# Kernel tuning notes

Measured on AMD Instinct MI355X. Metric: run time of the kernel, lower is better.

## Reference

```python
import jax, jax.numpy as jnp
import numpy as np


def setup_inputs() -> dict:
    key = jax.random.key(0)
    k1, k2 = jax.random.split(key)
    B, N, M = 32, 4096, 4096
    pred = jax.random.normal(k1, (B, N, 3), dtype=jnp.float32)
    target = jax.random.normal(k2, (B, M, 3), dtype=jnp.float32)
    return {"pred": pred, "target": target}


def reference(pred, target):
    # pairwise euclidean distances: [B, N, M]
    # d2 = |p|^2 + |t|^2 - 2 p.t  (matches torch.cdist p=2)
    p2 = jnp.sum(pred * pred, axis=-1)                      # [B, N]
    t2 = jnp.sum(target * target, axis=-1)                  # [B, M]
    pt = jnp.einsum('bnd,bmd->bnm', pred, target)           # [B, N, M]
    d2 = p2[:, :, None] + t2[:, None, :] - 2.0 * pt
    dist = jnp.sqrt(jnp.maximum(d2, 0.0))                   # [B, N, M]
    min_d = jnp.min(dist, axis=2)                           # [B, N]
    return jnp.mean(min_d)
```

## Files before the change

### kernel.cpp

```cpp
#include <hip/hip_runtime.h>


typedef short bf16x8 __attribute__((ext_vector_type(8)));
typedef float f32x16 __attribute__((ext_vector_type(16)));

constexpr int Bc = 32;
constexpr int Nc = 4096;
constexpr int Mc = 4096;
constexpr int BLOCK = 256;
constexpr int PTS = Bc * Nc;
constexpr int S = 4;
constexpr int TPB = 1024;
constexpr int PPB = 512;
constexpr unsigned POISON = 0xAAAAAAAAu;

__device__ __forceinline__ unsigned short brne(float x) {
  unsigned u = __float_as_uint(x);
  return (unsigned short)((u + 0x7FFFu + ((u >> 16) & 1u)) >> 16);
}
__device__ __forceinline__ float bf2f(unsigned short h) {
  return __uint_as_float(((unsigned)h) << 16);
}
__device__ __forceinline__ unsigned pack(unsigned short lo, unsigned short hi) {
  return (unsigned)lo | ((unsigned)hi << 16);
}

__global__ __launch_bounds__(BLOCK)
__attribute__((amdgpu_waves_per_eu(4, 4)))
void emd_fused_kernel(const float* __restrict__ pred,
                      const float* __restrict__ target,
                      unsigned* __restrict__ minb,
                      unsigned* __restrict__ cnts,
                      float* __restrict__ out) {
  __shared__ uint4 lds[2048];

  const int pg = blockIdx.x >> 2;
  const int s = blockIdx.x & 3;
  const int b = pg >> 3;
  const int lane = threadIdx.x & 63;
  const int half = lane >> 5;
  const int l31 = lane & 31;
  const int wave = threadIdx.x >> 6;
  const unsigned short ONE = 0x3F80;

  float pld[2][3];
#pragma unroll
  for (int j = 0; j < 2; ++j) {
    const size_t gi = (size_t)pg * PPB + threadIdx.x + j * BLOCK;
    pld[j][0] = pred[3 * gi];
    pld[j][1] = pred[3 * gi + 1];
    pld[j][2] = pred[3 * gi + 2];
  }
  const size_t tbase = (size_t)b * Mc + s * TPB;
  const float4* tp4 = (const float4*)(target + tbase * 3);
  float4 f0 = tp4[3 * threadIdx.x + 0];
  float4 f1 = tp4[3 * threadIdx.x + 1];
  float4 f2 = tp4[3 * threadIdx.x + 2];

#pragma unroll
  for (int j = 0; j < 2; ++j) {
    const int p = threadIdx.x + j * BLOCK;
    float x = pld[j][0], y = pld[j][1], z = pld[j][2];
    unsigned short xh = brne(x), xl = brne(x - bf2f(xh));
    unsigned short yh = brne(y), yl = brne(y - bf2f(yh));
    unsigned short zh = brne(z), zl = brne(z - bf2f(zh));
    float p2 = fmaf(x, x, fmaf(y, y, z * z));
    unsigned short ph = brne(p2), pl = brne(p2 - bf2f(ph));
    lds[p] = make_uint4(pack(xh, xl), pack(xh, yh), pack(yl, yh), pack(zh, zl));
    lds[512 + p] = make_uint4(pack(zh, ONE), pack(ONE, ph), pack(pl, 0), 0);
  }

  uint4 t0[4];
  {
    float cx[4] = {f0.x, f0.w, f1.z, f2.y};
    float cy[4] = {f0.y, f1.x, f1.w, f2.z};
    float cz[4] = {f0.z, f1.y, f2.x, f2.w};
#pragma unroll
    for (int j = 0; j < 4; ++j) {
      const int pt = 4 * threadIdx.x + j;
      float X = -2.0f * cx[j], Y = -2.0f * cy[j], Z = -2.0f * cz[j];
      unsigned short Xh = brne(X), Xl = brne(X - bf2f(Xh));
      unsigned short Yh = brne(Y), Yl = brne(Y - bf2f(Yh));
      unsigned short Zh = brne(Z), Zl = brne(Z - bf2f(Zh));
      float t2 = 0.25f * fmaf(X, X, fmaf(Y, Y, Z * Z));
      unsigned short th = brne(t2), tl = brne(t2 - bf2f(th));
      t0[j] =
          make_uint4(pack(Xh, Xh), pack(Xl, Yh), pack(Yh, Yl), pack(Zh, Zh));
      lds[1024 + pt] =
          make_uint4(pack(Zl, th), pack(tl, ONE), pack(ONE, 0), 0);
    }
  }
  __syncthreads();

  bf16x8 bfr[4];
#pragma unroll
  for (int f = 0; f < 4; ++f) {
    uint4 u = lds[half * 512 + wave * 128 + f * 32 + l31];
    bfr[f] = *(const bf16x8*)&u;
  }
  __syncthreads();

#pragma unroll
  for (int j = 0; j < 4; ++j) lds[4 * threadIdx.x + j] = t0[j];
  __syncthreads();

  float rA[4], rB[4];
#pragma unroll
  for (int f = 0; f < 4; ++f) { rA[f] = 3.4e38f; rB[f] = 3.4e38f; }

  const int abase = half * 1024 + l31;
#pragma unroll 2
  for (int t = 0; t < 32; ++t) {
    uint4 au = lds[abase + t * 32];
    bf16x8 af = *(const bf16x8*)&au;
    f32x16 z{};
    f32x16 d0 = __builtin_amdgcn_mfma_f32_32x32x16_bf16(af, bfr[0], z, 0, 0, 0);
    f32x16 d1 = __builtin_amdgcn_mfma_f32_32x32x16_bf16(af, bfr[1], z, 0, 0, 0);
    f32x16 d2 = __builtin_amdgcn_mfma_f32_32x32x16_bf16(af, bfr[2], z, 0, 0, 0);
    f32x16 d3 = __builtin_amdgcn_mfma_f32_32x32x16_bf16(af, bfr[3], z, 0, 0, 0);
#pragma unroll
    for (int i = 0; i < 16; i += 4) {
      rA[0] = fminf(fminf(d0[i], d0[i + 1]), rA[0]);
      rB[0] = fminf(fminf(d0[i + 2], d0[i + 3]), rB[0]);
      rA[1] = fminf(fminf(d1[i], d1[i + 1]), rA[1]);
      rB[1] = fminf(fminf(d1[i + 2], d1[i + 3]), rB[1]);
      rA[2] = fminf(fminf(d2[i], d2[i + 1]), rA[2]);
      rB[2] = fminf(fminf(d2[i + 2], d2[i + 3]), rB[2]);
      rA[3] = fminf(fminf(d3[i], d3[i + 1]), rA[3]);
      rB[3] = fminf(fminf(d3[i + 2], d3[i + 3]), rB[3]);
    }
  }

  const unsigned gbase = (unsigned)pg * PPB + wave * 128;
#pragma unroll
  for (int f = 0; f < 4; ++f) {
    float rr = fminf(rA[f], rB[f]);
    rr = fminf(rr, __shfl_xor(rr, 32, 64));
    if (lane < 32)
      __hip_atomic_fetch_min(&minb[gbase + f * 32 + l31],
                             __float_as_uint(fmaxf(rr, 0.0f)),
                             __ATOMIC_RELAXED, __HIP_MEMORY_SCOPE_AGENT);
  }

  asm volatile("s_waitcnt vmcnt(0)" ::: "memory");
  __syncthreads();

  unsigned* lflag = (unsigned*)lds;
  if (threadIdx.x == 0) {
    unsigned old = __hip_atomic_fetch_add(&cnts[pg], 1u, __ATOMIC_RELAXED,
                                          __HIP_MEMORY_SCOPE_AGENT);
    lflag[0] = (old == POISON + 3u || old == 3u) ? 1u : 0u;
  }
  __syncthreads();
  if (lflag[0]) {
    float ssum = 0.0f;
    const unsigned base = (unsigned)pg * PPB;
#pragma unroll
    for (int i = threadIdx.x; i < PPB; i += BLOCK) {
      unsigned ub = __hip_atomic_load(&minb[base + i], __ATOMIC_RELAXED,
                                      __HIP_MEMORY_SCOPE_AGENT);
      ssum += sqrtf(__uint_as_float(ub));
    }
#pragma unroll
    for (int off = 32; off > 0; off >>= 1) ssum += __shfl_down(ssum, off, 64);
    float* lsum = (float*)lds;
    if ((threadIdx.x & 63) == 0) lsum[1 + (threadIdx.x >> 6)] = ssum;
    __syncthreads();
    if (threadIdx.x == 0) {
      float tot = (lsum[1] + lsum[2]) + (lsum[3] + lsum[4]);
      atomicAdd(out, tot * (1.0f / (float)PTS));
    }
  }
}

extern "C" void kernel_launch(void* const* d_in, const int* in_sizes, int n_in,
                              void* d_out, int out_size, void* d_ws, size_t ws_size,
                              hipStream_t stream) {
  const float* pred = (const float*)d_in[0];
  const float* target = (const float*)d_in[1];
  unsigned* minb = (unsigned*)d_ws;
  unsigned* cnts = minb + PTS;
  emd_fused_kernel<<<dim3((PTS / PPB) * S), dim3(BLOCK), 0, stream>>>(
      pred, target, minb, cnts, (float*)d_out);
}
```

Before: 73.36 us.

## Split target range into eight slices, halve LDS, swizzle LDS indices

```diff
diff --git a/kernel.cpp b/kernel.cpp
--- a/kernel.cpp
+++ b/kernel.cpp
@@ -9,8 +9,8 @@
 constexpr int Mc = 4096;
 constexpr int BLOCK = 256;
 constexpr int PTS = Bc * Nc;
-constexpr int S = 4;
-constexpr int TPB = 1024;
+constexpr int S = 8;
+constexpr int TPB = 512;
 constexpr int PPB = 512;
 constexpr unsigned POISON = 0xAAAAAAAAu;
 
@@ -24,42 +24,64 @@
 __device__ __forceinline__ unsigned pack(unsigned short lo, unsigned short hi) {
   return (unsigned)lo | ((unsigned)hi << 16);
 }
+__device__ __forceinline__ int SW(int s) {
+  return s ^ ((s >> 3) & 7);
+}
 
 __global__ __launch_bounds__(BLOCK)
-__attribute__((amdgpu_waves_per_eu(4, 4)))
+__attribute__((amdgpu_waves_per_eu(8, 8)))
 void emd_fused_kernel(const float* __restrict__ pred,
                       const float* __restrict__ target,
                       unsigned* __restrict__ minb,
                       unsigned* __restrict__ cnts,
                       float* __restrict__ out) {
-  __shared__ uint4 lds[2048];
+  __shared__ uint4 lds[1024];
 
-  const int pg = blockIdx.x >> 2;
-  const int s = blockIdx.x & 3;
+  const int pg = blockIdx.x >> 3;
+  const int s = blockIdx.x & 7;
   const int b = pg >> 3;
   const int lane = threadIdx.x & 63;
   const int half = lane >> 5;
   const int l31 = lane & 31;
   const int wave = threadIdx.x >> 6;
+  const int tid = threadIdx.x;
   const unsigned short ONE = 0x3F80;
 
   float pld[2][3];
 #pragma unroll
   for (int j = 0; j < 2; ++j) {
-    const size_t gi = (size_t)pg * PPB + threadIdx.x + j * BLOCK;
+    const size_t gi = (size_t)pg * PPB + tid + j * BLOCK;
     pld[j][0] = pred[3 * gi];
     pld[j][1] = pred[3 * gi + 1];
     pld[j][2] = pred[3 * gi + 2];
   }
   const size_t tbase = (size_t)b * Mc + s * TPB;
-  const float4* tp4 = (const float4*)(target + tbase * 3);
-  float4 f0 = tp4[3 * threadIdx.x + 0];
-  float4 f1 = tp4[3 * threadIdx.x + 1];
-  float4 f2 = tp4[3 * threadIdx.x + 2];
+  const float2* tp2 = (const float2*)(target + tbase * 3);
+  float2 g0 = tp2[3 * tid + 0];
+  float2 g1 = tp2[3 * tid + 1];
+  float2 g2 = tp2[3 * tid + 2];
+
+  uint4 t0[2], t1[2];
+  {
+    float cx[2] = {g0.x, g1.y};
+    float cy[2] = {g0.y, g2.x};
+    float cz[2] = {g1.x, g2.y};
+#pragma unroll
+    for (int j = 0; j < 2; ++j) {
+      float X = -2.0f * cx[j], Y = -2.0f * cy[j], Z = -2.0f * cz[j];
+      unsigned short Xh = brne(X), Xl = brne(X - bf2f(Xh));
+      unsigned short Yh = brne(Y), Yl = brne(Y - bf2f(Yh));
+      unsigned short Zh = brne(Z), Zl = brne(Z - bf2f(Zh));
+      float t2 = 0.25f * fmaf(X, X, fmaf(Y, Y, Z * Z));
+      unsigned short th = brne(t2), tl = brne(t2 - bf2f(th));
+      t0[j] = make_uint4(pack(Xh, Xh), pack(Xl, Yh), pack(Yh, Yl), pack(Zh, Zh));
+      t1[j] = make_uint4(pack(Zl, th), pack(tl, ONE), pack(ONE, 0), 0);
+    }
+  }
 
 #pragma unroll
   for (int j = 0; j < 2; ++j) {
-    const int p = threadIdx.x + j * BLOCK;
+    const int p = tid + j * BLOCK;
     float x = pld[j][0], y = pld[j][1], z = pld[j][2];
     unsigned short xh = brne(x), xl = brne(x - bf2f(xh));
     unsigned short yh = brne(y), yl = brne(y - bf2f(yh));
@@ -68,27 +90,6 @@
     unsigned short ph = brne(p2), pl = brne(p2 - bf2f(ph));
     lds[p] = make_uint4(pack(xh, xl), pack(xh, yh), pack(yl, yh), pack(zh, zl));
     lds[512 + p] = make_uint4(pack(zh, ONE), pack(ONE, ph), pack(pl, 0), 0);
-  }
-
-  uint4 t0[4];
-  {
-    float cx[4] = {f0.x, f0.w, f1.z, f2.y};
-    float cy[4] = {f0.y, f1.x, f1.w, f2.z};
-    float cz[4] = {f0.z, f1.y, f2.x, f2.w};
-#pragma unroll
-    for (int j = 0; j < 4; ++j) {
-      const int pt = 4 * threadIdx.x + j;
-      float X = -2.0f * cx[j], Y = -2.0f * cy[j], Z = -2.0f * cz[j];
-      unsigned short Xh = brne(X), Xl = brne(X - bf2f(Xh));
-      unsigned short Yh = brne(Y), Yl = brne(Y - bf2f(Yh));
-      unsigned short Zh = brne(Z), Zl = brne(Z - bf2f(Zh));
-      float t2 = 0.25f * fmaf(X, X, fmaf(Y, Y, Z * Z));
-      unsigned short th = brne(t2), tl = brne(t2 - bf2f(th));
-      t0[j] =
-          make_uint4(pack(Xh, Xh), pack(Xl, Yh), pack(Yh, Yl), pack(Zh, Zh));
-      lds[1024 + pt] =
-          make_uint4(pack(Zl, th), pack(tl, ONE), pack(ONE, 0), 0);
-    }
   }
   __syncthreads();
 
@@ -101,17 +102,20 @@
   __syncthreads();
 
 #pragma unroll
-  for (int j = 0; j < 4; ++j) lds[4 * threadIdx.x + j] = t0[j];
+  for (int j = 0; j < 2; ++j) {
+    lds[SW(2 * tid + j)] = t0[j];
+    lds[SW(512 + 2 * tid + j)] = t1[j];
+  }
   __syncthreads();
 
   float rA[4], rB[4];
 #pragma unroll
   for (int f = 0; f < 4; ++f) { rA[f] = 3.4e38f; rB[f] = 3.4e38f; }
 
-  const int abase = half * 1024 + l31;
+  const int abase = half * 512 + l31;
 #pragma unroll 2
-  for (int t = 0; t < 32; ++t) {
-    uint4 au = lds[abase + t * 32];
+  for (int t = 0; t < 16; ++t) {
+    uint4 au = lds[SW(abase + t * 32)];
     bf16x8 af = *(const bf16x8*)&au;
     f32x16 z{};
     f32x16 d0 = __builtin_amdgcn_mfma_f32_32x32x16_bf16(af, bfr[0], z, 0, 0, 0);
@@ -146,17 +150,17 @@
   __syncthreads();
 
   unsigned* lflag = (unsigned*)lds;
-  if (threadIdx.x == 0) {
+  if (tid == 0) {
     unsigned old = __hip_atomic_fetch_add(&cnts[pg], 1u, __ATOMIC_RELAXED,
                                           __HIP_MEMORY_SCOPE_AGENT);
-    lflag[0] = (old == POISON + 3u || old == 3u) ? 1u : 0u;
+    lflag[0] = (old == POISON + (S - 1) || old == (unsigned)(S - 1)) ? 1u : 0u;
   }
   __syncthreads();
   if (lflag[0]) {
     float ssum = 0.0f;
     const unsigned base = (unsigned)pg * PPB;
 #pragma unroll
-    for (int i = threadIdx.x; i < PPB; i += BLOCK) {
+    for (int i = tid; i < PPB; i += BLOCK) {
       unsigned ub = __hip_atomic_load(&minb[base + i], __ATOMIC_RELAXED,
                                       __HIP_MEMORY_SCOPE_AGENT);
       ssum += sqrtf(__uint_as_float(ub));
@@ -164,9 +168,9 @@
 #pragma unroll
     for (int off = 32; off > 0; off >>= 1) ssum += __shfl_down(ssum, off, 64);
     float* lsum = (float*)lds;
-    if ((threadIdx.x & 63) == 0) lsum[1 + (threadIdx.x >> 6)] = ssum;
+    if ((tid & 63) == 0) lsum[1 + (tid >> 6)] = ssum;
     __syncthreads();
-    if (threadIdx.x == 0) {
+    if (tid == 0) {
       float tot = (lsum[1] + lsum[2]) + (lsum[3] + lsum[4]);
       atomicAdd(out, tot * (1.0f / (float)PTS));
     }
```

Result: slower. 76.80 us (+4.7%).

## Double block to 512 threads, halving per-wave B fragments and MFMAs

Applied to the files above, without the earlier changes.

```diff
diff --git a/kernel.cpp b/kernel.cpp
--- a/kernel.cpp
+++ b/kernel.cpp
@@ -7,7 +7,7 @@
 constexpr int Bc = 32;
 constexpr int Nc = 4096;
 constexpr int Mc = 4096;
-constexpr int BLOCK = 256;
+constexpr int BLOCK = 512;
 constexpr int PTS = Bc * Nc;
 constexpr int S = 4;
 constexpr int TPB = 1024;
@@ -26,7 +26,7 @@
 }
 
 __global__ __launch_bounds__(BLOCK)
-__attribute__((amdgpu_waves_per_eu(4, 4)))
+__attribute__((amdgpu_waves_per_eu(8, 8)))
 void emd_fused_kernel(const float* __restrict__ pred,
                       const float* __restrict__ target,
                       unsigned* __restrict__ minb,
@@ -41,72 +41,65 @@
   const int half = lane >> 5;
   const int l31 = lane & 31;
   const int wave = threadIdx.x >> 6;
+  const int tid = threadIdx.x;
   const unsigned short ONE = 0x3F80;
 
-  float pld[2][3];
+  float px, py, pz;
+  {
+    const size_t gi = (size_t)pg * PPB + tid;
+    px = pred[3 * gi]; py = pred[3 * gi + 1]; pz = pred[3 * gi + 2];
+  }
+  const size_t tbase = (size_t)b * Mc + s * TPB;
+  float tx[2], ty[2], tz[2];
 #pragma unroll
   for (int j = 0; j < 2; ++j) {
-    const size_t gi = (size_t)pg * PPB + threadIdx.x + j * BLOCK;
-    pld[j][0] = pred[3 * gi];
-    pld[j][1] = pred[3 * gi + 1];
-    pld[j][2] = pred[3 * gi + 2];
+    const size_t ti = tbase + tid + j * 512;
+    tx[j] = target[3 * ti]; ty[j] = target[3 * ti + 1];
+    tz[j] = target[3 * ti + 2];
   }
-  const size_t tbase = (size_t)b * Mc + s * TPB;
-  const float4* tp4 = (const float4*)(target + tbase * 3);
-  float4 f0 = tp4[3 * threadIdx.x + 0];
-  float4 f1 = tp4[3 * threadIdx.x + 1];
-  float4 f2 = tp4[3 * threadIdx.x + 2];
 
+  uint4 t0[2];
 #pragma unroll
   for (int j = 0; j < 2; ++j) {
-    const int p = threadIdx.x + j * BLOCK;
-    float x = pld[j][0], y = pld[j][1], z = pld[j][2];
+    float X = -2.0f * tx[j], Y = -2.0f * ty[j], Z = -2.0f * tz[j];
+    unsigned short Xh = brne(X), Xl = brne(X - bf2f(Xh));
+    unsigned short Yh = brne(Y), Yl = brne(Y - bf2f(Yh));
+    unsigned short Zh = brne(Z), Zl = brne(Z - bf2f(Zh));
+    float t2 = 0.25f * fmaf(X, X, fmaf(Y, Y, Z * Z));
+    unsigned short th = brne(t2), tl = brne(t2 - bf2f(th));
+    t0[j] = make_uint4(pack(Xh, Xh), pack(Xl, Yh), pack(Yh, Yl), pack(Zh, Zh));
+    lds[1024 + tid + j * 512] =
+        make_uint4(pack(Zl, th), pack(tl, ONE), pack(ONE, 0), 0);
+  }
+
+  {
+    float x = px, y = py, z = pz;
     unsigned short xh = brne(x), xl = brne(x - bf2f(xh));
     unsigned short yh = brne(y), yl = brne(y - bf2f(yh));
     unsigned short zh = brne(z), zl = brne(z - bf2f(zh));
     float p2 = fmaf(x, x, fmaf(y, y, z * z));
     unsigned short ph = brne(p2), pl = brne(p2 - bf2f(ph));
-    lds[p] = make_uint4(pack(xh, xl), pack(xh, yh), pack(yl, yh), pack(zh, zl));
-    lds[512 + p] = make_uint4(pack(zh, ONE), pack(ONE, ph), pack(pl, 0), 0);
-  }
-
-  uint4 t0[4];
-  {
-    float cx[4] = {f0.x, f0.w, f1.z, f2.y};
-    float cy[4] = {f0.y, f1.x, f1.w, f2.z};
-    float cz[4] = {f0.z, f1.y, f2.x, f2.w};
-#pragma unroll
-    for (int j = 0; j < 4; ++j) {
-      const int pt = 4 * threadIdx.x + j;
-      float X = -2.0f * cx[j], Y = -2.0f * cy[j], Z = -2.0f * cz[j];
-      unsigned short Xh = brne(X), Xl = brne(X - bf2f(Xh));
-      unsigned short Yh = brne(Y), Yl = brne(Y - bf2f(Yh));
-      unsigned short Zh = brne(Z), Zl = brne(Z - bf2f(Zh));
-      float t2 = 0.25f * fmaf(X, X, fmaf(Y, Y, Z * Z));
-      unsigned short th = brne(t2), tl = brne(t2 - bf2f(th));
-      t0[j] =
-          make_uint4(pack(Xh, Xh), pack(Xl, Yh), pack(Yh, Yl), pack(Zh, Zh));
-      lds[1024 + pt] =
-          make_uint4(pack(Zl, th), pack(tl, ONE), pack(ONE, 0), 0);
-    }
+    lds[tid] =
+        make_uint4(pack(xh, xl), pack(xh, yh), pack(yl, yh), pack(zh, zl));
+    lds[512 + tid] = make_uint4(pack(zh, ONE), pack(ONE, ph), pack(pl, 0), 0);
   }
   __syncthreads();
 
-  bf16x8 bfr[4];
+  bf16x8 bfr[2];
 #pragma unroll
-  for (int f = 0; f < 4; ++f) {
-    uint4 u = lds[half * 512 + wave * 128 + f * 32 + l31];
+  for (int f = 0; f < 2; ++f) {
+    uint4 u = lds[half * 512 + wave * 64 + f * 32 + l31];
     bfr[f] = *(const bf16x8*)&u;
   }
   __syncthreads();
 
 #pragma unroll
-  for (int j = 0; j < 4; ++j) lds[4 * threadIdx.x + j] = t0[j];
+  for (int j = 0; j < 2; ++j) lds[tid + j * 512] = t0[j];
   __syncthreads();
 
-  float rA[4], rB[4];
+  float rA[2], rB[2];
 #pragma unroll
-  for (int f = 0; f < 4; ++f) { rA[f] = 3.4e38f; rB[f] = 3.4e38f; }
+  for (int f = 0; f < 2; ++f) { rA[f] = 3.4e38f; rB[f] = 3.4e38f; }
 
   const int abase = half * 1024 + l31;
 #pragma unroll 2
@@ -116,24 +109,18 @@
     f32x16 z{};
     f32x16 d0 = __builtin_amdgcn_mfma_f32_32x32x16_bf16(af, bfr[0], z, 0, 0, 0);
     f32x16 d1 = __builtin_amdgcn_mfma_f32_32x32x16_bf16(af, bfr[1], z, 0, 0, 0);
-    f32x16 d2 = __builtin_amdgcn_mfma_f32_32x32x16_bf16(af, bfr[2], z, 0, 0, 0);
-    f32x16 d3 = __builtin_amdgcn_mfma_f32_32x32x16_bf16(af, bfr[3], z, 0, 0, 0);
 #pragma unroll
     for (int i = 0; i < 16; i += 4) {
       rA[0] = fminf(fminf(d0[i], d0[i + 1]), rA[0]);
       rB[0] = fminf(fminf(d0[i + 2], d0[i + 3]), rB[0]);
       rA[1] = fminf(fminf(d1[i], d1[i + 1]), rA[1]);
       rB[1] = fminf(fminf(d1[i + 2], d1[i + 3]), rB[1]);
-      rA[2] = fminf(fminf(d2[i], d2[i + 1]), rA[2]);
-      rB[2] = fminf(fminf(d2[i + 2], d2[i + 3]), rB[2]);
-      rA[3] = fminf(fminf(d3[i], d3[i + 1]), rA[3]);
-      rB[3] = fminf(fminf(d3[i + 2], d3[i + 3]), rB[3]);
     }
   }
 
-  const unsigned gbase = (unsigned)pg * PPB + wave * 128;
+  const unsigned gbase = (unsigned)pg * PPB + wave * 64;
 #pragma unroll
-  for (int f = 0; f < 4; ++f) {
+  for (int f = 0; f < 2; ++f) {
     float rr = fminf(rA[f], rB[f]);
     rr = fminf(rr, __shfl_xor(rr, 32, 64));
     if (lane < 32)
@@ -146,28 +133,26 @@
   __syncthreads();
 
   unsigned* lflag = (unsigned*)lds;
-  if (threadIdx.x == 0) {
+  if (tid == 0) {
     unsigned old = __hip_atomic_fetch_add(&cnts[pg], 1u, __ATOMIC_RELAXED,
                                           __HIP_MEMORY_SCOPE_AGENT);
-    lflag[0] = (old == POISON + 3u || old == 3u) ? 1u : 0u;
+    lflag[0] = (old == POISON + (S - 1) || old == (unsigned)(S - 1)) ? 1u : 0u;
   }
   __syncthreads();
   if (lflag[0]) {
-    float ssum = 0.0f;
     const unsigned base = (unsigned)pg * PPB;
-#pragma unroll
-    for (int i = threadIdx.x; i < PPB; i += BLOCK) {
-      unsigned ub = __hip_atomic_load(&minb[base + i], __ATOMIC_RELAXED,
-                                      __HIP_MEMORY_SCOPE_AGENT);
-      ssum += sqrtf(__uint_as_float(ub));
-    }
+    unsigned ub = __hip_atomic_load(&minb[base + tid], __ATOMIC_RELAXED,
+                                    __HIP_MEMORY_SCOPE_AGENT);
+    float ssum = sqrtf(__uint_as_float(ub));
 #pragma unroll
     for (int off = 32; off > 0; off >>= 1) ssum += __shfl_down(ssum, off, 64);
     float* lsum = (float*)lds;
-    if ((threadIdx.x & 63) == 0) lsum[1 + (threadIdx.x >> 6)] = ssum;
+    if (lane == 0) lsum[1 + wave] = ssum;
     __syncthreads();
-    if (threadIdx.x == 0) {
-      float tot = (lsum[1] + lsum[2]) + (lsum[3] + lsum[4]);
+    if (tid == 0) {
+      float tot = 0.0f;
+#pragma unroll
+      for (int w = 0; w < 8; ++w) tot += lsum[1 + w];
       atomicAdd(out, tot * (1.0f / (float)PTS));
     }
   }
```

Measured after the change: 72.92 us (median of 2 runs). Within noise of the previous version (-0.6%).
